# Kernel tuning notes

Hardware: AMD Instinct MI355X
Metric: run time of the kernel (lower is better)

## Reference

```python
import jax, jax.numpy as jnp
import numpy as np

# ---- constants mirroring the module config ----
TIMESTEPS = 1000
N_GT = 3            # GT phases {stable, pre-shock, shock}
NUM_EXPERTS = 6     # 2 sub-experts per GT phase; phase L -> experts {L, L+3}
LAMBDA_REG = 0.01
LAMBDA_LB = 0.01
PHASE_WEIGHTS = np.array([1.0, 5.0, 5.0], dtype=np.float32)


def _sinusoidal_embed(t, dim):
    # standard DDPM sinusoidal timestep embedding -> [B, dim]
    half = dim // 2
    freqs = jnp.exp(-jnp.log(10000.0) * jnp.arange(half, dtype=jnp.float32) / half)
    args = t.astype(jnp.float32)[:, None] * freqs[None, :]
    return jnp.concatenate([jnp.sin(args), jnp.cos(args)], axis=-1)


def _alphas_bar():
    betas = jnp.linspace(1e-4, 0.02, TIMESTEPS, dtype=jnp.float32)
    return jnp.cumprod(1.0 - betas)


def setup_inputs() -> dict:
    B, Tp, Tf, Df, Ds, dm, E, H = 512, 256, 64, 64, 32, 512, NUM_EXPERTS, 512
    key = jax.random.key(0)
    ks = jax.random.split(key, 16)
    s = 0.02  # init scale
    d_in = Df + 2 * dm  # noisy features + global ctx + t embedding
    return {
        'observed_data': jax.random.normal(ks[0], (B, Tp, Df), jnp.float32),
        'future_data':   jax.random.normal(ks[1], (B, Tf, Df), jnp.float32),
        'static_context': jax.random.normal(ks[2], (B, Ds), jnp.float32),
        'eps':           jax.random.normal(ks[3], (B, Tf, Df), jnp.float32),
        'phase_label':   jax.random.randint(ks[4], (B,), 0, N_GT),
        't':             jax.random.randint(ks[5], (B,), 0, TIMESTEPS),
        'W_enc':    jax.random.normal(ks[6], (Df, dm), jnp.float32) * s,
        'b_enc':    jnp.zeros((dm,), jnp.float32),
        'W_stat':   jax.random.normal(ks[7], (Ds, dm), jnp.float32) * s,
        'W_router': jax.random.normal(ks[8], (dm, E), jnp.float32) * s,
        'b_router': jnp.zeros((E,), jnp.float32),
        'W1': jax.random.normal(ks[9],  (E, d_in, H), jnp.float32) * s,
        'b1': jnp.zeros((E, H), jnp.float32),
        'W2': jax.random.normal(ks[10], (E, H, Df), jnp.float32) * s,
        'b2': jnp.zeros((E, Df), jnp.float32),
    }


def reference(observed_data, future_data, static_context, eps,
              W_enc, b_enc, W_stat, W_router, b_router,
              W1, b1, W2, b2, phase_label, t):
    B, Tf, Df = future_data.shape
    E = W1.shape[0]
    dm = W_enc.shape[1]

    # ---- frozen encoder (torch.no_grad in the original) ----
    ctx_seq = jax.nn.gelu(observed_data @ W_enc + (static_context @ W_stat)[:, None, :] + b_enc)  # [B,Tp,dm]
    global_ctx = ctx_seq.mean(axis=1)                                                             # [B,dm]
    ctx_seq = jax.lax.stop_gradient(ctx_seq)
    global_ctx = jax.lax.stop_gradient(global_ctx)

    # ---- router (trainable) ----
    router_logits = global_ctx @ W_router + b_router        # [B,E]
    router_probs = jax.nn.softmax(router_logits, axis=-1)

    # ---- GT-masked top-1 routing: phase p -> argmax over experts {p, p+3} ----
    selected = jnp.zeros((B,), jnp.int32)
    for p in range(N_GT):
        sub = jnp.stack([router_probs[:, p], router_probs[:, p + N_GT]], axis=1)  # [B,2]
        winner = p + N_GT * jnp.argmax(sub, axis=1).astype(jnp.int32)
        selected = jnp.where(phase_label == p, winner, selected)

    # ---- diffusion scheduler: add_noise ----
    ab = _alphas_bar()[t]                                   # [B]
    noisy_fut = (jnp.sqrt(ab)[:, None, None] * future_data
                 + jnp.sqrt(1.0 - ab)[:, None, None] * eps)  # [B,Tf,Df]

    # ---- expert backbones: run all E experts densely, then gather routed output ----
    t_emb = _sinusoidal_embed(t, dm)                        # [B,dm]
    cond = jnp.concatenate([
        noisy_fut,
        jnp.broadcast_to(global_ctx[:, None, :], (B, Tf, dm)),
        jnp.broadcast_to(t_emb[:, None, :],      (B, Tf, dm)),
    ], axis=-1)                                             # [B,Tf,Din]
    h = jax.nn.gelu(jnp.einsum('btd,edh->ebth', cond, W1) + b1[:, None, None, :])
    outputs_all = jnp.einsum('ebth,ehf->ebtf', h, W2) + b2[:, None, None, :]  # [E,B,Tf,Df]

    pred = outputs_all[selected, jnp.arange(B)]             # [B,Tf,Df] gradient-surgery dispatch
    loss_raw = jnp.mean((pred - eps) ** 2, axis=(1, 2))     # per-sample MSE, [B]

    # weighted_loss * count/B summed over experts == mean(loss_raw * w[selected%3])
    lw = jnp.asarray(PHASE_WEIGHTS)
    w_sample = lw[selected % N_GT]
    total_loss = jnp.mean(loss_raw * w_sample)

    # ---- consistency regularization on a fixed 4-sample subset ----
    S = min(B, 4)
    out_sub = outputs_all[:, :S]                            # [E,S,Tf,Df]
    chain = jnp.float32(0.0)
    for i in [0, 1, 3, 4]:
        if i + 1 < E:
            chain += jnp.mean((out_sub[i] - out_sub[i + 1]) ** 2)
    for i in range(N_GT):
        if i + N_GT < E:
            chain += jnp.mean((out_sub[i] - out_sub[i + N_GT]) ** 2)
    diff = out_sub[:, :, 1:] - out_sub[:, :, :-1]
    smooth = jnp.sum(jnp.mean(diff ** 2, axis=(1, 2, 3)))
    total_loss += (chain + 0.5 * smooth) * LAMBDA_REG

    # ---- load-balance loss ----
    onehot = (selected[:, None] == jnp.arange(E)[None, :]).astype(jnp.float32)  # [B,E]
    f = onehot.mean(axis=0)
    P = router_probs.mean(axis=0)
    total_loss += LAMBDA_LB * E * jnp.sum(f * P)

    return total_loss
```

## Files before the change

kernel.cpp:

```cpp
#include <hip/hip_runtime.h>

typedef float  f32x4 __attribute__((ext_vector_type(4)));
typedef short  s16x8 __attribute__((ext_vector_type(8)));
typedef unsigned short u16;
typedef u16    u16x4 __attribute__((ext_vector_type(4)));

#define TIMESTEPS 1000

#define WS_ALPHAS   0
#define WS_FREQS    1024
#define WS_PROBS    1536
#define WS_SELECTED 4608
#define WS_LOSSB    5632
#define WS_META     6144
#define WS_ROWSRC   6400
#define WS_ROWDST   7040
#define WS_PARTS    7680
#define WS_XC       270336
#define WS_HSTAT    532480
#define WS_HSTAT2   794624
#define WS_OUTSUB   806912
#define WS_U16BYTE  3620864
#define WS_BIAS     2691072
#define U_WENCT     0
#define U_W1T       32768
#define U_W2T       3375104

__device__ __forceinline__ u16 f2bf(float x){
    unsigned u = __builtin_bit_cast(unsigned, x);
    unsigned r = (u + 0x7FFFu + ((u >> 16) & 1u)) >> 16;
    return (u16)r;
}

__device__ __forceinline__ float gelu_f(float x){
    float x2 = x * x;
    float t  = x * fmaf(0.035677408136f, x2, 0.7978845608028654f);
    float ex = __builtin_amdgcn_exp2f(t * 2.885390081777927f);
    float r  = __builtin_amdgcn_rcpf(ex + 1.0f);
    return fmaf(-x, r, x);
}

__device__ __forceinline__ void mfma16(f32x4& c, s16x8 a, s16x8 b){
    asm volatile("v_mfma_f32_16x16x32_bf16 %0, %1, %2, %0" : "+v"(c) : "v"(a), "v"(b));
}

__global__ __launch_bounds__(256) void k0T(const float* __restrict__ Wenc,
                                           const float* __restrict__ W1,
                                           const float* __restrict__ W2,
                                           const float* __restrict__ stat,
                                           const float* __restrict__ Wstat,
                                           const float* __restrict__ benc,
                                           u16* __restrict__ uws,
                                           float* __restrict__ ws){
    __shared__ float sT[32][33];
    int bid = blockIdx.x, tid = threadIdx.x;
    const int t1 = 6*34*16, t2 = t1 + 6*16*2, t3 = t2 + 2*16;
    if(bid == t3){
        __shared__ float sp[256];
        for(int k = tid; k < 256; k += 256)
            ws[WS_FREQS + k] = expf(-logf(10000.0f) * (float)k / 256.0f);
        float p = 1.f;
        #pragma unroll
        for(int r = 0; r < 4; r++){
            int i = tid*4 + r;
            if(i < TIMESTEPS){
                float beta = 0.0001f + (0.02f - 0.0001f) * ((float)i / 999.0f);
                p *= (1.0f - beta);
            }
        }
        sp[tid] = p;
        __syncthreads();
        for(int st = 1; st < 256; st <<= 1){
            float v = (tid >= st) ? sp[tid - st] : 1.0f;
            __syncthreads();
            sp[tid] *= v;
            __syncthreads();
        }
        float run = (tid == 0) ? 1.0f : sp[tid - 1];
        for(int r = 0; r < 4; r++){
            int i = tid*4 + r;
            if(i < TIMESTEPS){
                float beta = 0.0001f + (0.02f - 0.0001f) * ((float)i / 999.0f);
                run *= (1.0f - beta);
                ws[WS_ALPHAS + i] = run;
            }
        }
        return;
    }
    if(bid > t3){
        __shared__ float sSt[8*32];
        int g = bid - t3 - 1;
        int b0 = g*8;
        sSt[tid & 255] = stat[b0*32 + (tid & 255)];
        __syncthreads();
        #pragma unroll
        for(int half = 0; half < 2; half++){
            int j = tid + half*256;
            float acc[8] = {0,0,0,0,0,0,0,0};
            for(int s = 0; s < 32; s++){
                float wv = Wstat[s*512 + j];
                #pragma unroll
                for(int bb = 0; bb < 8; bb++) acc[bb] += sSt[bb*32 + s] * wv;
            }
            float bz = benc[j];
            #pragma unroll
            for(int bb = 0; bb < 8; bb++)
                ws[WS_BIAS + (b0 + bb)*512 + j] = acc[bb] + bz;
        }
        return;
    }
    const float* src; u16* dst; int K, J, kt, jt;
    if(bid < t1){
        int e = bid / 544, r = bid % 544; kt = r / 16; jt = r % 16;
        src = W1 + (size_t)e*1088*512; dst = uws + U_W1T + (size_t)e*512*1088; K = 1088; J = 512;
    } else if(bid < t2){
        int r = bid - t1; int e = r / 32; r %= 32; kt = r / 2; jt = r % 2;
        src = W2 + (size_t)e*512*64; dst = uws + U_W2T + (size_t)e*64*512; K = 512; J = 64;
    } else {
        int r = bid - t2; kt = r / 16; jt = r % 16;
        src = Wenc; dst = uws + U_WENCT; K = 64; J = 512;
    }
    int ty = tid >> 5, tx = tid & 31;
    #pragma unroll
    for(int i = 0; i < 4; i++)
        sT[ty + i*8][tx] = src[(size_t)(kt*32 + ty + i*8)*J + jt*32 + tx];
    __syncthreads();
    #pragma unroll
    for(int i = 0; i < 4; i++)
        dst[(size_t)(jt*32 + ty + i*8)*K + kt*32 + tx] = f2bf(sT[tx][ty + i*8]);
}

#define PADX 72
__global__ __launch_bounds__(512) void k1_enc(const float* __restrict__ obs,
        const u16* __restrict__ uws, const float* __restrict__ Wr,
        const float* __restrict__ br, const int* __restrict__ phase,
        const int* __restrict__ t_arr, float* __restrict__ ws){
    __shared__ u16  sX[256 * PADX];
    __shared__ float sBias[512];
    __shared__ float sG[512];
    __shared__ float sRed[8][6];
    int b = blockIdx.x, tid = threadIdx.x;
    {
        int row = tid >> 1, c0 = (tid & 1) * 32;
        const f32x4* src = (const f32x4*)&obs[((size_t)b*256 + row)*64 + c0];
        u16* dst = &sX[row*PADX + c0];
        #pragma unroll
        for(int i = 0; i < 8; i++){
            f32x4 v = src[i];
            u16x4 pk; pk.x = f2bf(v.x); pk.y = f2bf(v.y); pk.z = f2bf(v.z); pk.w = f2bf(v.w);
            *(u16x4*)(dst + i*4) = pk;
        }
    }
    sBias[tid] = ws[WS_BIAS + b*512 + tid];
    __syncthreads();
    int w = tid >> 6, l = tid & 63, lr = l & 15, lk = (l >> 4) * 8;
    const u16* wencT = uws + U_WENCT;
    s16x8 bf[4][2];
    float bias[4];
    #pragma unroll
    for(int n = 0; n < 4; n++){
        int col = w*64 + n*16 + lr;
        bf[n][0] = *(const s16x8*)&wencT[col*64 + lk];
        bf[n][1] = *(const s16x8*)&wencT[col*64 + 32 + lk];
        bias[n]  = sBias[col];
    }
    float cac[4] = {0.f, 0.f, 0.f, 0.f};
    for(int mt = 0; mt < 16; mt++){
        s16x8 a0 = *(const s16x8*)&sX[(mt*16 + lr)*PADX + lk];
        s16x8 a1 = *(const s16x8*)&sX[(mt*16 + lr)*PADX + 32 + lk];
        #pragma unroll
        for(int n = 0; n < 4; n++){
            f32x4 acc = {bias[n], bias[n], bias[n], bias[n]};
            mfma16(acc, a0, bf[n][0]);
            mfma16(acc, a1, bf[n][1]);
            cac[n] += gelu_f(acc.x) + gelu_f(acc.y) + gelu_f(acc.z) + gelu_f(acc.w);
        }
    }
    #pragma unroll
    for(int n = 0; n < 4; n++){
        cac[n] += __shfl_xor(cac[n], 16);
        cac[n] += __shfl_xor(cac[n], 32);
    }
    if(l < 16){
        #pragma unroll
        for(int n = 0; n < 4; n++)
            sG[w*64 + n*16 + l] = cac[n] * (1.0f/256.0f);
    }
    __syncthreads();
    float gv = sG[tid];
    u16* XC = (u16*)(ws + WS_XC);
    XC[b*1024 + tid] = f2bf(gv);
    int tv = t_arr[b];
    {
        float fr = ws[WS_FREQS + (tid & 255)];
        float ang = (float)tv * fr;
        XC[b*1024 + 512 + tid] = f2bf((tid < 256) ? sinf(ang) : cosf(ang));
    }
    float p6[6];
    #pragma unroll
    for(int e = 0; e < 6; e++) p6[e] = gv * Wr[tid*6 + e];
    #pragma unroll
    for(int off = 32; off > 0; off >>= 1)
        #pragma unroll
        for(int e = 0; e < 6; e++) p6[e] += __shfl_down(p6[e], off);
    if(l == 0)
        #pragma unroll
        for(int e = 0; e < 6; e++) sRed[w][e] = p6[e];
    __syncthreads();
    if(tid == 0){
        float logit[6], mx = -1e30f;
        #pragma unroll
        for(int e = 0; e < 6; e++){
            float s = 0.f;
            #pragma unroll
            for(int q = 0; q < 8; q++) s += sRed[q][e];
            logit[e] = s + br[e];
            mx = fmaxf(mx, logit[e]);
        }
        float s = 0.f, p[6];
        #pragma unroll
        for(int e = 0; e < 6; e++){ p[e] = expf(logit[e] - mx); s += p[e]; }
        float inv = 1.0f / s;
        #pragma unroll
        for(int e = 0; e < 6; e++) ws[WS_PROBS + b*6 + e] = p[e] * inv;
        int ph = phase[b];
        int sel = ph + ((logit[ph + 3] > logit[ph]) ? 3 : 0);
        ((int*)ws)[WS_SELECTED + b] = sel;
    }
}

__global__ __launch_bounds__(512) void k2b_group(float* __restrict__ ws){
    __shared__ int sCnt[8][6];
    __shared__ int sBase[8][6];
    __shared__ int sSec[6], sTot[6];
    int tid = threadIdx.x, w = tid >> 6, l = tid & 63;
    int* wsi = (int*)ws;
    int sv = wsi[WS_SELECTED + tid];
    unsigned long long mym = 0;
    #pragma unroll
    for(int e = 0; e < 6; e++){
        unsigned long long m = __ballot(sv == e);
        if(l == 0) sCnt[w][e] = __popcll(m);
        if(sv == e) mym = m;
    }
    __syncthreads();
    if(tid == 0){
        int o = 0;
        for(int e = 0; e < 6; e++){
            sSec[e] = o;
            int t0 = 0;
            for(int ww = 0; ww < 8; ww++){ sBase[ww][e] = o; o += sCnt[ww][e]; t0 += sCnt[ww][e]; }
            sTot[e] = t0;
            o += 4;
        }
        int nch = 0;
        for(int e = 0; e < 6; e++){
            int len = sTot[e] + 4, st = sSec[e];
            for(int s = 0; s < len; s += 64){
                int cl = len - s; if(cl > 64) cl = 64;
                wsi[WS_META + 4 + nch*4 + 0] = e;
                wsi[WS_META + 4 + nch*4 + 1] = st + s;
                wsi[WS_META + 4 + nch*4 + 2] = cl;
                nch++;
            }
        }
        wsi[WS_META] = nch;
    }
    __syncthreads();
    int rank = __popcll(mym & ((1ull << l) - 1ull));
    int pos = sBase[w][sv] + rank;
    wsi[WS_ROWSRC + pos] = tid;
    wsi[WS_ROWDST + pos] = WS_HSTAT + tid*512;
    if(tid < 24){
        int e = tid >> 2, b = tid & 3;
        int pos2 = sSec[e] + sTot[e] + b;
        wsi[WS_ROWSRC + pos2] = b;
        wsi[WS_ROWDST + pos2] = WS_HSTAT2 + (e*4 + b)*512;
    }
}

__global__ __launch_bounds__(256) void k3_hstat(const u16* __restrict__ uws,
        const float* __restrict__ b1, float* __restrict__ ws){
    __shared__ int sSrc[64], sDst[64];
    int bid = blockIdx.x, tid = threadIdx.x;
    int c = bid >> 3, jt = bid & 7;
    int* wsi = (int*)ws;
    if(c >= wsi[WS_META]) return;
    int e    = wsi[WS_META + 4 + c*4 + 0];
    int start= wsi[WS_META + 4 + c*4 + 1];
    int len  = wsi[WS_META + 4 + c*4 + 2];
    if(tid < 64){
        int ok = tid < len;
        sSrc[tid] = ok ? wsi[WS_ROWSRC + start + tid] : 0;
        sDst[tid] = ok ? wsi[WS_ROWDST + start + tid] : -1;
    }
    __syncthreads();
    int w = tid >> 6, l = tid & 63, lr = l & 15, lk = (l >> 4) * 8;
    int col = jt*64 + w*16 + lr;
    const u16* XC = (const u16*)(ws + WS_XC);
    const u16* rowA[4];
    #pragma unroll
    for(int mt = 0; mt < 4; mt++)
        rowA[mt] = XC + (size_t)sSrc[mt*16 + lr]*1024 + lk;
    const u16* bp = uws + U_W1T + ((size_t)e*512 + col)*1088 + 64 + lk;
    f32x4 acc[4];
    {
        float bv = b1[e*512 + col];
        f32x4 z = {bv, bv, bv, bv};
        #pragma unroll
        for(int mt = 0; mt < 4; mt++) acc[mt] = z;
    }
    #pragma unroll 4
    for(int ks = 0; ks < 32; ks++){
        s16x8 bb = *(const s16x8*)(bp + ks*32);
        s16x8 a0 = *(const s16x8*)(rowA[0] + ks*32);
        s16x8 a1 = *(const s16x8*)(rowA[1] + ks*32);
        s16x8 a2 = *(const s16x8*)(rowA[2] + ks*32);
        s16x8 a3 = *(const s16x8*)(rowA[3] + ks*32);
        mfma16(acc[0], a0, bb);
        mfma16(acc[1], a1, bb);
        mfma16(acc[2], a2, bb);
        mfma16(acc[3], a3, bb);
    }
    #pragma unroll
    for(int mt = 0; mt < 4; mt++){
        #pragma unroll
        for(int rg = 0; rg < 4; rg++){
            int r = mt*16 + (l >> 4)*4 + rg;
            int d = sDst[r];
            if(d >= 0) ws[d + col] = acc[mt][rg];
        }
    }
}

#define PADN 72
#define PADH 520
__global__ __launch_bounds__(512) void k4_ffn(const float* __restrict__ fut,
        const float* __restrict__ eps, const int* __restrict__ t_arr,
        const u16* __restrict__ uws, const float* __restrict__ b2,
        float* __restrict__ ws){
    __shared__ u16 sN[64 * PADN];
    __shared__ u16 sH[64 * PADH];
    __shared__ float sHs[512];
    __shared__ float sRed[8];
    int tid = threadIdx.x, bid = blockIdx.x;
    int* wsi = (int*)ws;
    int b, e, store;
    if(bid < 512){ b = bid; e = wsi[WS_SELECTED + b]; store = 0; }
    else { int r = bid - 512; e = r >> 2; b = r & 3; store = 1; }
    sHs[tid] = store ? ws[WS_HSTAT2 + (e*4 + b)*512 + tid] : ws[WS_HSTAT + b*512 + tid];
    int tv = t_arr[b];
    float ab = ws[WS_ALPHAS + tv];
    float sa = sqrtf(ab), sb = sqrtf(1.0f - ab);
    {
        int r = tid >> 3, c0 = (tid & 7) * 8;
        const f32x4* pf = (const f32x4*)&fut[((size_t)b*64 + r)*64 + c0];
        const f32x4* pe = (const f32x4*)&eps[((size_t)b*64 + r)*64 + c0];
        f32x4 f0 = pf[0], f1 = pf[1], e0 = pe[0], e1 = pe[1];
        u16x4 p0, p1;
        p0.x = f2bf(sa*f0.x + sb*e0.x); p0.y = f2bf(sa*f0.y + sb*e0.y);
        p0.z = f2bf(sa*f0.z + sb*e0.z); p0.w = f2bf(sa*f0.w + sb*e0.w);
        p1.x = f2bf(sa*f1.x + sb*e1.x); p1.y = f2bf(sa*f1.y + sb*e1.y);
        p1.z = f2bf(sa*f1.z + sb*e1.z); p1.w = f2bf(sa*f1.w + sb*e1.w);
        *(u16x4*)&sN[r*PADN + c0]     = p0;
        *(u16x4*)&sN[r*PADN + c0 + 4] = p1;
    }
    __syncthreads();
    int w = tid >> 6, l = tid & 63, lr = l & 15, lk = (l >> 4) * 8;
    const u16* w1T = uws + U_W1T;
    const u16* w2T = uws + U_W2T;
    s16x8 aw[4][2];
    #pragma unroll
    for(int mt = 0; mt < 4; mt++){
        int jrow = w*64 + mt*16 + lr;
        aw[mt][0] = *(const s16x8*)&w1T[((size_t)e*512 + jrow)*1088 + lk];
        aw[mt][1] = *(const s16x8*)&w1T[((size_t)e*512 + jrow)*1088 + 32 + lk];
    }
    #pragma unroll
    for(int nt = 0; nt < 4; nt++){
        s16x8 nb0 = *(const s16x8*)&sN[(nt*16 + lr)*PADN + lk];
        s16x8 nb1 = *(const s16x8*)&sN[(nt*16 + lr)*PADN + 32 + lk];
        #pragma unroll
        for(int mt = 0; mt < 4; mt++){
            int j0 = w*64 + mt*16 + (l >> 4)*4;
            f32x4 acc = *(const f32x4*)&sHs[j0];
            mfma16(acc, aw[mt][0], nb0);
            mfma16(acc, aw[mt][1], nb1);
            u16x4 pk;
            pk.x = f2bf(gelu_f(acc.x)); pk.y = f2bf(gelu_f(acc.y));
            pk.z = f2bf(gelu_f(acc.z)); pk.w = f2bf(gelu_f(acc.w));
            *(u16x4*)&sH[(nt*16 + lr)*PADH + j0] = pk;
        }
    }
    __syncthreads();
    int mtg = (w >> 2) << 1;
    int nt  = w & 3;
    f32x4 oacc[2];
    {
        float bz = b2[e*64 + nt*16 + lr];
        f32x4 z = {bz, bz, bz, bz}; oacc[0] = z; oacc[1] = z;
    }
    for(int ks = 0; ks < 16; ks++){
        s16x8 bb = *(const s16x8*)&w2T[((size_t)e*64 + nt*16 + lr)*512 + ks*32 + lk];
        #pragma unroll
        for(int i = 0; i < 2; i++){
            s16x8 a = *(const s16x8*)&sH[((mtg + i)*16 + lr)*PADH + ks*32 + lk];
            mfma16(oacc[i], a, bb);
        }
    }
    if(store){
        #pragma unroll
        for(int i = 0; i < 2; i++)
            #pragma unroll
            for(int rg = 0; rg < 4; rg++){
                int row = (mtg + i)*16 + (l >> 4)*4 + rg;
                int col = nt*16 + lr;
                ws[WS_OUTSUB + (e*4 + b)*4096 + row*64 + col] = oacc[i][rg];
            }
    } else {
        float ls = 0.f;
        #pragma unroll
        for(int i = 0; i < 2; i++)
            #pragma unroll
            for(int rg = 0; rg < 4; rg++){
                int row = (mtg + i)*16 + (l >> 4)*4 + rg;
                int col = nt*16 + lr;
                float d = oacc[i][rg] - eps[((size_t)b*64 + row)*64 + col];
                ls += d*d;
            }
        #pragma unroll
        for(int off = 32; off > 0; off >>= 1) ls += __shfl_down(ls, off);
        if(l == 0) sRed[w] = ls;
        __syncthreads();
        if(tid == 0){
            float s = 0.f;
            #pragma unroll
            for(int q = 0; q < 8; q++) s += sRed[q];
            const float pw[3] = {1.f, 5.f, 5.f};
            ws[WS_LOSSB + b] = (s * (1.0f/4096.0f)) * pw[e % 3];
        }
    }
}

__global__ __launch_bounds__(256) void k5a_parts(float* __restrict__ ws){
    __shared__ float red[256];
    int bid = blockIdx.x, tid = threadIdx.x;
    float s = 0.f;
    if(bid < 7){
        const int pa[7] = {0,1,3,4,0,1,2};
        const int pb[7] = {1,2,4,5,3,4,5};
        const float* A  = &ws[WS_OUTSUB + pa[bid]*16384];
        const float* Bp = &ws[WS_OUTSUB + pb[bid]*16384];
        for(int i = tid; i < 4096; i += 256){
            f32x4 a = *(const f32x4*)&A[i*4];
            f32x4 c = *(const f32x4*)&Bp[i*4];
            f32x4 d = a - c;
            s += d.x*d.x + d.y*d.y + d.z*d.z + d.w*d.w;
        }
        s *= (1.0f/16384.0f);
    } else {
        int e = bid - 7;
        const float* O = &ws[WS_OUTSUB + e*16384];
        for(int i = tid; i < 4*63*16; i += 256){
            int sm = i / (63*16); int r = i % (63*16);
            int tf = r / 16; int f4 = (r % 16) * 4;
            f32x4 a = *(const f32x4*)&O[(sm*64 + tf + 1)*64 + f4];
            f32x4 c = *(const f32x4*)&O[(sm*64 + tf)*64 + f4];
            f32x4 d = a - c;
            s += d.x*d.x + d.y*d.y + d.z*d.z + d.w*d.w;
        }
        s *= (1.0f/16128.0f) * 0.5f;
    }
    red[tid] = s;
    __syncthreads();
    for(int st = 128; st > 0; st >>= 1){
        if(tid < st) red[tid] += red[tid + st];
        __syncthreads();
    }
    if(tid == 0) ws[WS_PARTS + bid] = red[0];
}

__global__ __launch_bounds__(512) void k5b_final(float* __restrict__ ws, float* __restrict__ out){
    __shared__ float sW[8];
    __shared__ float sF[8][6], sP[8][6];
    int tid = threadIdx.x, w = tid >> 6, l = tid & 63;
    int* wsi = (int*)ws;
    int sel = wsi[WS_SELECTED + tid];
    float lv = ws[WS_LOSSB + tid];
    float pv[6], cf[6];
    #pragma unroll
    for(int e = 0; e < 6; e++){
        pv[e] = ws[WS_PROBS + tid*6 + e];
        cf[e] = (sel == e) ? 1.f : 0.f;
    }
    #pragma unroll
    for(int off = 32; off > 0; off >>= 1){
        lv += __shfl_down(lv, off);
        #pragma unroll
        for(int e = 0; e < 6; e++){
            pv[e] += __shfl_down(pv[e], off);
            cf[e] += __shfl_down(cf[e], off);
        }
    }
    if(l == 0){
        sW[w] = lv;
        #pragma unroll
        for(int e = 0; e < 6; e++){ sF[w][e] = cf[e]; sP[w][e] = pv[e]; }
    }
    __syncthreads();
    if(tid == 0){
        float total = 0.f;
        for(int q = 0; q < 8; q++) total += sW[q];
        total *= (1.0f/512.0f);
        float reg = 0.f;
        for(int p = 0; p < 13; p++) reg += ws[WS_PARTS + p];
        total += 0.01f * reg;
        float lb = 0.f;
        for(int e = 0; e < 6; e++){
            float f = 0.f, pp = 0.f;
            for(int q = 0; q < 8; q++){ f += sF[q][e]; pp += sP[q][e]; }
            lb += (f * (1.0f/512.f)) * (pp * (1.0f/512.f));
        }
        out[0] = total + 0.01f * 6.0f * lb;
    }
}

extern "C" void kernel_launch(void* const* d_in, const int* in_sizes, int n_in,
                              void* d_out, int out_size, void* d_ws, size_t ws_size,
                              hipStream_t stream){
    const float* obs  = (const float*)d_in[0];
    const float* fut  = (const float*)d_in[1];
    const float* stat = (const float*)d_in[2];
    const float* eps  = (const float*)d_in[3];
    const int*   phase= (const int*)d_in[4];
    const int*   t    = (const int*)d_in[5];
    const float* Wenc = (const float*)d_in[6];
    const float* benc = (const float*)d_in[7];
    const float* Wstat= (const float*)d_in[8];
    const float* Wr   = (const float*)d_in[9];
    const float* br   = (const float*)d_in[10];
    const float* W1   = (const float*)d_in[11];
    const float* b1   = (const float*)d_in[12];
    const float* W2   = (const float*)d_in[13];
    const float* b2   = (const float*)d_in[14];
    float* ws  = (float*)d_ws;
    u16*   uws = (u16*)((char*)d_ws + WS_U16BYTE);
    float* out = (float*)d_out;

    k0T<<<3553, 256, 0, stream>>>(Wenc, W1, W2, stat, Wstat, benc, uws, ws);
    k1_enc<<<512, 512, 0, stream>>>(obs, uws, Wr, br, phase, t, ws);
    k2b_group<<<1, 512, 0, stream>>>(ws);
    k3_hstat<<<112, 256, 0, stream>>>(uws, b1, ws);
    k4_ffn<<<536, 512, 0, stream>>>(fut, eps, t, uws, b2, ws);
    k5a_parts<<<13, 256, 0, stream>>>(ws);
    k5b_final<<<1, 512, 0, stream>>>(ws, out);
}
```

Before: 105.3 us.

## Fuse grouping into hstat kernel and merge final reductions via atomic flag

Result: no change. 104.1 us (median of 2 runs) (-1.2%).

```diff
diff --git a/kernel.cpp b/kernel.cpp
--- a/kernel.cpp
+++ b/kernel.cpp
@@ -12,10 +12,8 @@
 #define WS_PROBS    1536
 #define WS_SELECTED 4608
 #define WS_LOSSB    5632
-#define WS_META     6144
-#define WS_ROWSRC   6400
-#define WS_ROWDST   7040
 #define WS_PARTS    7680
+#define WS_FLAG     7700
 #define WS_XC       270336
 #define WS_HSTAT    532480
 #define WS_HSTAT2   794624
@@ -229,73 +227,69 @@
     }
 }
 
-__global__ __launch_bounds__(512) void k2b_group(float* __restrict__ ws){
-    __shared__ int sCnt[8][6];
-    __shared__ int sBase[8][6];
-    __shared__ int sSec[6], sTot[6];
-    int tid = threadIdx.x, w = tid >> 6, l = tid & 63;
+__global__ __launch_bounds__(256) void k3_hstat(const u16* __restrict__ uws,
+        const float* __restrict__ b1, float* __restrict__ ws){
+    __shared__ int sSrc[64], sDst[64];
+    __shared__ int sCnt[8][6], sBase[8][6], sSec[6], sTot[6];
+    __shared__ int sChunk[16][3];
+    __shared__ int sNch;
+    int bid = blockIdx.x, tid = threadIdx.x;
+    int w = tid >> 6, l = tid & 63;
     int* wsi = (int*)ws;
-    int sv = wsi[WS_SELECTED + tid];
-    unsigned long long mym = 0;
+    if(bid == 0 && tid == 0) wsi[WS_FLAG] = 0;
+    int sv0 = wsi[WS_SELECTED + tid];
+    int sv1 = wsi[WS_SELECTED + 256 + tid];
+    unsigned long long mym0 = 0, mym1 = 0;
     #pragma unroll
     for(int e = 0; e < 6; e++){
-        unsigned long long m = __ballot(sv == e);
-        if(l == 0) sCnt[w][e] = __popcll(m);
-        if(sv == e) mym = m;
-    }
+        unsigned long long m0 = __ballot(sv0 == e);
+        unsigned long long m1 = __ballot(sv1 == e);
+        if(l == 0){ sCnt[w][e] = __popcll(m0); sCnt[4 + w][e] = __popcll(m1); }
+        if(sv0 == e) mym0 = m0;
+        if(sv1 == e) mym1 = m1;
+    }
+    if(tid < 64){ sSrc[tid] = 0; sDst[tid] = -1; }
     __syncthreads();
     if(tid == 0){
         int o = 0;
         for(int e = 0; e < 6; e++){
-            sSec[e] = o;
-            int t0 = 0;
-            for(int ww = 0; ww < 8; ww++){ sBase[ww][e] = o; o += sCnt[ww][e]; t0 += sCnt[ww][e]; }
-            sTot[e] = t0;
-            o += 4;
+            sSec[e] = o; int t0 = 0;
+            for(int g = 0; g < 8; g++){ sBase[g][e] = o; o += sCnt[g][e]; t0 += sCnt[g][e]; }
+            sTot[e] = t0; o += 4;
         }
         int nch = 0;
         for(int e = 0; e < 6; e++){
             int len = sTot[e] + 4, st = sSec[e];
             for(int s = 0; s < len; s += 64){
-                int cl = len - s; if(cl > 64) cl = 64;
-                wsi[WS_META + 4 + nch*4 + 0] = e;
-                wsi[WS_META + 4 + nch*4 + 1] = st + s;
-                wsi[WS_META + 4 + nch*4 + 2] = cl;
-                nch++;
-            }
-        }
-        wsi[WS_META] = nch;
-    }
-    __syncthreads();
-    int rank = __popcll(mym & ((1ull << l) - 1ull));
-    int pos = sBase[w][sv] + rank;
-    wsi[WS_ROWSRC + pos] = tid;
-    wsi[WS_ROWDST + pos] = WS_HSTAT + tid*512;
+                sChunk[nch][0] = e; sChunk[nch][1] = st + s;
+                sChunk[nch][2] = (len - s < 64) ? (len - s) : 64; nch++;
+            }
+        }
+        sNch = nch;
+    }
+    __syncthreads();
+    int c = bid >> 3, jt = bid & 7;
+    if(c >= sNch) return;
+    int e     = sChunk[c][0];
+    int start = sChunk[c][1];
+    int len   = sChunk[c][2];
+    {
+        int rank = __popcll(mym0 & ((1ull << l) - 1ull));
+        int pos = sBase[w][sv0] + rank - start;
+        if(pos >= 0 && pos < len){ sSrc[pos] = tid; sDst[pos] = WS_HSTAT + tid*512; }
+    }
+    {
+        int rank = __popcll(mym1 & ((1ull << l) - 1ull));
+        int pos = sBase[4 + w][sv1] + rank - start;
+        if(pos >= 0 && pos < len){ sSrc[pos] = 256 + tid; sDst[pos] = WS_HSTAT + (256 + tid)*512; }
+    }
     if(tid < 24){
-        int e = tid >> 2, b = tid & 3;
-        int pos2 = sSec[e] + sTot[e] + b;
-        wsi[WS_ROWSRC + pos2] = b;
-        wsi[WS_ROWDST + pos2] = WS_HSTAT2 + (e*4 + b)*512;
-    }
-}
-
-__global__ __launch_bounds__(256) void k3_hstat(const u16* __restrict__ uws,
-        const float* __restrict__ b1, float* __restrict__ ws){
-    __shared__ int sSrc[64], sDst[64];
-    int bid = blockIdx.x, tid = threadIdx.x;
-    int c = bid >> 3, jt = bid & 7;
-    int* wsi = (int*)ws;
-    if(c >= wsi[WS_META]) return;
-    int e    = wsi[WS_META + 4 + c*4 + 0];
-    int start= wsi[WS_META + 4 + c*4 + 1];
-    int len  = wsi[WS_META + 4 + c*4 + 2];
-    if(tid < 64){
-        int ok = tid < len;
-        sSrc[tid] = ok ? wsi[WS_ROWSRC + start + tid] : 0;
-        sDst[tid] = ok ? wsi[WS_ROWDST + start + tid] : -1;
-    }
-    __syncthreads();
-    int w = tid >> 6, l = tid & 63, lr = l & 15, lk = (l >> 4) * 8;
+        int ea = tid >> 2, ba = tid & 3;
+        int pos = sSec[ea] + sTot[ea] + ba - start;
+        if(pos >= 0 && pos < len){ sSrc[pos] = ba; sDst[pos] = WS_HSTAT2 + (ea*4 + ba)*512; }
+    }
+    __syncthreads();
+    int lr = l & 15, lk = (l >> 4) * 8;
     int col = jt*64 + w*16 + lr;
     const u16* XC = (const u16*)(ws + WS_XC);
     const u16* rowA[4];
@@ -346,8 +340,8 @@
     int tid = threadIdx.x, bid = blockIdx.x;
     int* wsi = (int*)ws;
     int b, e, store;
-    if(bid < 512){ b = bid; e = wsi[WS_SELECTED + b]; store = 0; }
-    else { int r = bid - 512; e = r >> 2; b = r & 3; store = 1; }
+    if(bid < 24){ e = bid >> 2; b = bid & 3; store = 1; }
+    else { b = bid - 24; e = wsi[WS_SELECTED + b]; store = 0; }
     sHs[tid] = store ? ws[WS_HSTAT2 + (e*4 + b)*512 + tid] : ws[WS_HSTAT + b*512 + tid];
     int tv = t_arr[b];
     float ab = ws[WS_ALPHAS + tv];
@@ -442,56 +436,66 @@
     }
 }
 
-__global__ __launch_bounds__(256) void k5a_parts(float* __restrict__ ws){
-    __shared__ float red[256];
+__global__ __launch_bounds__(256) void k5_final(float* __restrict__ ws, float* __restrict__ out){
     int bid = blockIdx.x, tid = threadIdx.x;
-    float s = 0.f;
-    if(bid < 7){
-        const int pa[7] = {0,1,3,4,0,1,2};
-        const int pb[7] = {1,2,4,5,3,4,5};
-        const float* A  = &ws[WS_OUTSUB + pa[bid]*16384];
-        const float* Bp = &ws[WS_OUTSUB + pb[bid]*16384];
-        for(int i = tid; i < 4096; i += 256){
-            f32x4 a = *(const f32x4*)&A[i*4];
-            f32x4 c = *(const f32x4*)&Bp[i*4];
-            f32x4 d = a - c;
-            s += d.x*d.x + d.y*d.y + d.z*d.z + d.w*d.w;
-        }
-        s *= (1.0f/16384.0f);
-    } else {
-        int e = bid - 7;
-        const float* O = &ws[WS_OUTSUB + e*16384];
-        for(int i = tid; i < 4*63*16; i += 256){
-            int sm = i / (63*16); int r = i % (63*16);
-            int tf = r / 16; int f4 = (r % 16) * 4;
-            f32x4 a = *(const f32x4*)&O[(sm*64 + tf + 1)*64 + f4];
-            f32x4 c = *(const f32x4*)&O[(sm*64 + tf)*64 + f4];
-            f32x4 d = a - c;
-            s += d.x*d.x + d.y*d.y + d.z*d.z + d.w*d.w;
-        }
-        s *= (1.0f/16128.0f) * 0.5f;
-    }
-    red[tid] = s;
-    __syncthreads();
-    for(int st = 128; st > 0; st >>= 1){
-        if(tid < st) red[tid] += red[tid + st];
+    int* wsi = (int*)ws;
+    if(bid < 13){
+        __shared__ float red[256];
+        float s = 0.f;
+        if(bid < 7){
+            const int pa[7] = {0,1,3,4,0,1,2};
+            const int pb[7] = {1,2,4,5,3,4,5};
+            const float* A  = &ws[WS_OUTSUB + pa[bid]*16384];
+            const float* Bp = &ws[WS_OUTSUB + pb[bid]*16384];
+            for(int i = tid; i < 4096; i += 256){
+                f32x4 a = *(const f32x4*)&A[i*4];
+                f32x4 c = *(const f32x4*)&Bp[i*4];
+                f32x4 d = a - c;
+                s += d.x*d.x + d.y*d.y + d.z*d.z + d.w*d.w;
+            }
+            s *= (1.0f/16384.0f);
+        } else {
+            int e = bid - 7;
+            const float* O = &ws[WS_OUTSUB + e*16384];
+            for(int i = tid; i < 4*63*16; i += 256){
+                int sm = i / (63*16); int r = i % (63*16);
+                int tf = r / 16; int f4 = (r % 16) * 4;
+                f32x4 a = *(const f32x4*)&O[(sm*64 + tf + 1)*64 + f4];
+                f32x4 c = *(const f32x4*)&O[(sm*64 + tf)*64 + f4];
+                f32x4 d = a - c;
+                s += d.x*d.x + d.y*d.y + d.z*d.z + d.w*d.w;
+            }
+            s *= (1.0f/16128.0f) * 0.5f;
+        }
+        red[tid] = s;
         __syncthreads();
-    }
-    if(tid == 0) ws[WS_PARTS + bid] = red[0];
-}
-
-__global__ __launch_bounds__(512) void k5b_final(float* __restrict__ ws, float* __restrict__ out){
-    __shared__ float sW[8];
-    __shared__ float sF[8][6], sP[8][6];
-    int tid = threadIdx.x, w = tid >> 6, l = tid & 63;
-    int* wsi = (int*)ws;
-    int sel = wsi[WS_SELECTED + tid];
-    float lv = ws[WS_LOSSB + tid];
+        for(int st = 128; st > 0; st >>= 1){
+            if(tid < st) red[tid] += red[tid + st];
+            __syncthreads();
+        }
+        if(tid == 0){
+            ws[WS_PARTS + bid] = red[0];
+            __threadfence();
+            atomicAdd(&wsi[WS_FLAG], 1);
+        }
+        return;
+    }
+    if(tid == 0){
+        while(atomicAdd(&wsi[WS_FLAG], 0) < 13) __builtin_amdgcn_s_sleep(2);
+    }
+    __syncthreads();
+    __threadfence();
+    __shared__ float sW[4];
+    __shared__ float sF[4][6], sP[4][6];
+    int w = tid >> 6, l = tid & 63;
+    int sel0 = wsi[WS_SELECTED + tid];
+    int sel1 = wsi[WS_SELECTED + 256 + tid];
+    float lv = ws[WS_LOSSB + tid] + ws[WS_LOSSB + 256 + tid];
     float pv[6], cf[6];
     #pragma unroll
     for(int e = 0; e < 6; e++){
-        pv[e] = ws[WS_PROBS + tid*6 + e];
-        cf[e] = (sel == e) ? 1.f : 0.f;
+        pv[e] = ws[WS_PROBS + tid*6 + e] + ws[WS_PROBS + (256 + tid)*6 + e];
+        cf[e] = ((sel0 == e) ? 1.f : 0.f) + ((sel1 == e) ? 1.f : 0.f);
     }
     #pragma unroll
     for(int off = 32; off > 0; off >>= 1){
@@ -510,15 +514,16 @@
     __syncthreads();
     if(tid == 0){
         float total = 0.f;
-        for(int q = 0; q < 8; q++) total += sW[q];
+        for(int q = 0; q < 4; q++) total += sW[q];
         total *= (1.0f/512.0f);
+        volatile float* vp = ws + WS_PARTS;
         float reg = 0.f;
-        for(int p = 0; p < 13; p++) reg += ws[WS_PARTS + p];
+        for(int p = 0; p < 13; p++) reg += vp[p];
         total += 0.01f * reg;
         float lb = 0.f;
         for(int e = 0; e < 6; e++){
             float f = 0.f, pp = 0.f;
-            for(int q = 0; q < 8; q++){ f += sF[q][e]; pp += sP[q][e]; }
+            for(int q = 0; q < 4; q++){ f += sF[q][e]; pp += sP[q][e]; }
             lb += (f * (1.0f/512.f)) * (pp * (1.0f/512.f));
         }
         out[0] = total + 0.01f * 6.0f * lb;
@@ -549,9 +554,7 @@
 
     k0T<<<3553, 256, 0, stream>>>(Wenc, W1, W2, stat, Wstat, benc, uws, ws);
     k1_enc<<<512, 512, 0, stream>>>(obs, uws, Wr, br, phase, t, ws);
-    k2b_group<<<1, 512, 0, stream>>>(ws);
     k3_hstat<<<112, 256, 0, stream>>>(uws, b1, ws);
     k4_ffn<<<536, 512, 0, stream>>>(fut, eps, t, uws, b2, ws);
-    k5a_parts<<<13, 256, 0, stream>>>(ws);
-    k5b_final<<<1, 512, 0, stream>>>(ws, out);
-}
+    k5_final<<<14, 256, 0, stream>>>(ws, out);
+}
```
